# Kernel tuning notes

Hardware: AMD Instinct MI355X
Metric: run time of the kernel (lower is better)

The kernel has to match this reference:

```python
import jax, jax.numpy as jnp
import numpy as np


def _conv1x1(x, w, b):
    # x: (B, C, H, W), w: (O, C), b: (O,)  -> (B, O, H, W)
    return jnp.einsum('oc,bchw->bohw', w, x) + b[None, :, None, None]


def _branch(xq, xkv, wq, bq, wk, bk, wv, bv):
    B, C, H, W = xq.shape
    N = H * W
    q = _conv1x1(xq, wq, bq).reshape(B, -1, N)   # (B, d, N)
    k = _conv1x1(xkv, wk, bk).reshape(B, -1, N)  # (B, d, N)
    v = _conv1x1(xkv, wv, bv).reshape(B, C, N)   # (B, C, N)
    energy = jnp.einsum('bdi,bdj->bij', q, k)    # (B, N, N), no scale (as in source)
    attn = jax.nn.softmax(energy, axis=-1)
    out = jnp.einsum('bcj,bij->bci', v, attn)    # bmm(v, attn^T)
    return out.reshape(B, C, H, W)


def setup_inputs() -> dict:
    key = jax.random.key(0)
    ks = jax.random.split(key, 16)
    B, C, H, W = 4, 256, 64, 64
    d = C // 8
    s_in = 0.02
    inp = {
        'x1': jax.random.normal(ks[0], (B, C, H, W), jnp.float32),
        'x2': jax.random.normal(ks[1], (B, C, H, W), jnp.float32),
        'wq1': jax.random.normal(ks[2], (d, C), jnp.float32) * s_in,
        'bq1': jnp.zeros((d,), jnp.float32),
        'wk1': jax.random.normal(ks[3], (d, C), jnp.float32) * s_in,
        'bk1': jnp.zeros((d,), jnp.float32),
        'wv1': jax.random.normal(ks[4], (C, C), jnp.float32) * s_in,
        'bv1': jnp.zeros((C,), jnp.float32),
        'wq2': jax.random.normal(ks[5], (d, C), jnp.float32) * s_in,
        'bq2': jnp.zeros((d,), jnp.float32),
        'wk2': jax.random.normal(ks[6], (d, C), jnp.float32) * s_in,
        'bk2': jnp.zeros((d,), jnp.float32),
        'wv2': jax.random.normal(ks[7], (C, C), jnp.float32) * s_in,
        'bv2': jnp.zeros((C,), jnp.float32),
    }
    return inp


def reference(x1, x2, wq1, bq1, wk1, bk1, wv1, bv1, wq2, bq2, wk2, bk2, wv2, bv2):
    out1 = _branch(x1, x2, wq1, bq1, wk1, bk1, wv1, bv1)
    out2 = _branch(x1, x2, wq2, bq2, wk2, bk2, wv2, bv2)
    return x1 + x2 + out1 + out2
```

## Files before the change

kernel.cpp:

```cpp
#include <hip/hip_runtime.h>
#include <hip/hip_fp8.h>

#define N_TOK 4096
#define C_DIM 256
#define D_DIM 32

typedef float f32x4 __attribute__((ext_vector_type(4)));
typedef short short8 __attribute__((ext_vector_type(8)));
typedef unsigned short u16;
typedef unsigned char u8;
typedef long long i64;

__device__ __forceinline__ u16 f2bf(float f) {
    unsigned int u = __builtin_bit_cast(unsigned int, f);
    u += 0x7fffu + ((u >> 16) & 1u);
    return (u16)(u >> 16);
}
__device__ __forceinline__ float bf2f(u16 h) {
    unsigned int u = ((unsigned int)h) << 16;
    return __builtin_bit_cast(float, u);
}
__device__ __forceinline__ float exp2_fast(float x) {
#if __has_builtin(__builtin_amdgcn_exp2f)
    return __builtin_amdgcn_exp2f(x);
#else
    return exp2f(x);
#endif
}
template<bool HI>
__device__ __forceinline__ int pk_fp8(float a, float b, int old) {
#if __has_builtin(__builtin_amdgcn_cvt_pk_fp8_f32)
    return __builtin_amdgcn_cvt_pk_fp8_f32(a, b, old, HI);
#else
    __hip_fp8_e4m3 fa(a), fb(b);
    int v = (int)fa.__x | ((int)fb.__x << 8);
    return HI ? ((old & 0xffff) | (v << 16)) : ((old & ~0xffff) | (v & 0xffff));
#endif
}
__device__ __forceinline__ u8 f2fp8(float f) {
    return (u8)(pk_fp8<false>(f, f, 0) & 0xff);
}


__global__ __launch_bounds__(256) void qk_proj(
    const float* __restrict__ x1, const float* __restrict__ x2,
    const float* __restrict__ wq1, const float* __restrict__ bq1,
    const float* __restrict__ wk1, const float* __restrict__ bk1,
    const float* __restrict__ wq2, const float* __restrict__ bq2,
    const float* __restrict__ wk2, const float* __restrict__ bk2,
    u16* __restrict__ wsQ, u16* __restrict__ wsK)
{
    __shared__ float w_lds[32 * 256];
    const int ib = blockIdx.x;
    const int comb = blockIdx.y;
    const int b = comb & 3;
    const int branch = (comb >> 2) & 1;
    const int qk = comb >> 3;

    const float* x = qk ? x2 : x1;
    const float* w; const float* bias; u16* dst;
    if (qk == 0) { w = branch ? wq2 : wq1; bias = branch ? bq2 : bq1; dst = wsQ; }
    else         { w = branch ? wk2 : wk1; bias = branch ? bk2 : bk1; dst = wsK; }
    const int slice = branch * 4 + b;
    dst += (size_t)slice * N_TOK * D_DIM;
    const float osc = (qk == 0) ? 1.44269504088896341f : 1.0f;

    const int tid = threadIdx.x;
    for (int t = tid; t < 32 * 256; t += 256) w_lds[t] = w[t];
    __syncthreads();

    const int il = tid & 63;
    const int db = tid >> 6;
    const float* xc = x + (size_t)b * C_DIM * N_TOK + ib * 64 + il;

    float acc[8] = {0.f,0.f,0.f,0.f,0.f,0.f,0.f,0.f};
    for (int c4 = 0; c4 < 256; c4 += 4) {
        const float xv0 = xc[(size_t)(c4 + 0) * N_TOK];
        const float xv1 = xc[(size_t)(c4 + 1) * N_TOK];
        const float xv2 = xc[(size_t)(c4 + 2) * N_TOK];
        const float xv3 = xc[(size_t)(c4 + 3) * N_TOK];
#pragma unroll
        for (int mm = 0; mm < 8; ++mm) {
            const float4 wv = *(const float4*)&w_lds[(db * 8 + mm) * 256 + c4];
            acc[mm] += xv0 * wv.x + xv1 * wv.y + xv2 * wv.z + xv3 * wv.w;
        }
    }
    short8 pack;
#pragma unroll
    for (int mm = 0; mm < 8; ++mm)
        pack[mm] = (short)f2bf((acc[mm] + bias[db * 8 + mm]) * osc);
    *(short8*)(dst + (size_t)(ib * 64 + il) * D_DIM + db * 8) = pack;
}

__device__ __forceinline__ void stage_xt(u16* xtb, const float* xb, int ks,
                                         int wave, int lane)
{
    const int j  = (wave & 1) * 64 + lane;
    const int cb = (wave >> 1) * 16;
    const float* xp = xb + (size_t)(ks * 32 + cb) * N_TOK + j;
    u16 vals[16];
#pragma unroll
    for (int qq = 0; qq < 16; ++qq) vals[qq] = f2bf(xp[(size_t)qq * N_TOK]);
    const int swz = (j >> 1) & 3;
    u16* row = xtb + j * 32;
    const int c0 = cb >> 3;
    *(short8*)&row[((c0    ) ^ swz) * 8] = *(const short8*)&vals[0];
    *(short8*)&row[((c0 + 1) ^ swz) * 8] = *(const short8*)&vals[8];
}

__global__ __launch_bounds__(256, 2) void v_proj(
    const float* __restrict__ x2,
    const float* __restrict__ wv1, const float* __restrict__ bv1,
    const float* __restrict__ wv2, const float* __restrict__ bv2,
    u8* __restrict__ wsV)
{
    __shared__ __align__(16) u16 wl[128 * 256];
    __shared__ __align__(16) u16 xt[2][128 * 32];

    const int jt = blockIdx.x, ct = blockIdx.y, s = blockIdx.z;
    const int branch = s >> 2, b = s & 3;
    const float* w    = branch ? wv2 : wv1;
    const float* bias = branch ? bv2 : bv1;
    u8* dstB = wsV + (size_t)s * N_TOK * C_DIM;
    const float* xb = x2 + (size_t)b * C_DIM * N_TOK + jt * 128;

    const int tid = threadIdx.x;
    const int wave = tid >> 6, lane = tid & 63;
    const int wr = wave >> 1, wc = wave & 1;
    const int g = lane >> 4, li = lane & 15;

    {
        const int c = tid >> 1;
        const int kh = (tid & 1) * 128;
        const float* wrow = w + (size_t)(ct * 128 + c) * C_DIM + kh;
        u16* lrow = wl + c * 256;
#pragma unroll
        for (int kk = 0; kk < 128; kk += 8) {
            const float4 a0 = *(const float4*)&wrow[kk];
            const float4 a1 = *(const float4*)&wrow[kk + 4];
            u16 tmp[8] = {f2bf(a0.x), f2bf(a0.y), f2bf(a0.z), f2bf(a0.w),
                          f2bf(a1.x), f2bf(a1.y), f2bf(a1.z), f2bf(a1.w)};
            const int kc = (kh + kk) >> 3;
            *(short8*)&lrow[(kc ^ (c & 7)) * 8] = *(const short8*)tmp;
        }
    }
    stage_xt(&xt[0][0], xb, 0, wave, lane);
    __syncthreads();

    f32x4 acc[4][4];
#pragma unroll
    for (int mf = 0; mf < 4; ++mf)
#pragma unroll
        for (int nf = 0; nf < 4; ++nf) acc[mf][nf] = (f32x4){0.f, 0.f, 0.f, 0.f};

    int buf = 0;
    for (int ks = 0; ks < 8; ++ks) {
        if (ks < 7) stage_xt(&xt[buf ^ 1][0], xb, ks + 1, wave, lane);

        short8 af[4], bf[4];
#pragma unroll
        for (int mf = 0; mf < 4; ++mf) {
            const int c = wr * 64 + mf * 16 + li;
            af[mf] = *(const short8*)&wl[c * 256 + (((ks * 4 + g) ^ (li & 7)) * 8)];
        }
#pragma unroll
        for (int nf = 0; nf < 4; ++nf) {
            const int j = wc * 64 + nf * 16 + li;
            bf[nf] = *(const short8*)&xt[buf][j * 32 + ((g ^ ((j >> 1) & 3)) * 8)];
        }
        __builtin_amdgcn_s_setprio(1);
#pragma unroll
        for (int mf = 0; mf < 4; ++mf)
#pragma unroll
            for (int nf = 0; nf < 4; ++nf)
                acc[mf][nf] = __builtin_amdgcn_mfma_f32_16x16x32_bf16(
                    af[mf], bf[nf], acc[mf][nf], 0, 0, 0);
        __builtin_amdgcn_s_setprio(0);
        __syncthreads();
        buf ^= 1;
    }

#pragma unroll
    for (int mf = 0; mf < 4; ++mf) {
#pragma unroll
        for (int r = 0; r < 4; ++r) {
            const int c = ct * 128 + wr * 64 + mf * 16 + 4 * g + r;
            const float bv = bias[c];
#pragma unroll
            for (int nf = 0; nf < 4; ++nf) {
                const int j = jt * 128 + wc * 64 + nf * 16 + li;
                dstB[(size_t)(j >> 5) * 8192 + ((j >> 3) & 3) * 2048
                     + c * 8 + (j & 7)] = f2fp8(acc[mf][nf][r] + bv);
            }
        }
    }
}

__global__ __launch_bounds__(256, 4) void attn_fwd(
    const u16* __restrict__ Q, const u16* __restrict__ K,
    const u8* __restrict__ V, u16* __restrict__ O)
{
    __shared__ __align__(16) u8 vlds[2][2][4096];
    __shared__ float lscr[2][2][64][2];

    const int n  = blockIdx.x;
    const int s  = n & 7;
    const int ib = (n >> 3) & 63;
    const int ct = n >> 9;
    const u16* q = Q + (size_t)s * N_TOK * D_DIM;
    const u16* k = K + (size_t)s * N_TOK * D_DIM;
    const u8*  v = V + (size_t)s * N_TOK * C_DIM + ct * 1024;
    u16*       o = O + (size_t)s * N_TOK * C_DIM + ct * 128;

    const int tid  = threadIdx.x;
    const int wave = tid >> 6;
    const int lane = tid & 63;
    const int grp  = wave >> 1;
    const int wg   = wave & 1;
    const int g    = lane >> 4;
    const int li   = lane & 15;
    const int i0   = ib * 64 + wg * 32;
    const int jbase = grp * (N_TOK / 2);
    const int NP = N_TOK / 2 / 32;

    short8 qf[2];
    qf[0] = *(const short8*)(q + (size_t)(i0 + li) * D_DIM + 8 * g);
    qf[1] = *(const short8*)(q + (size_t)(i0 + 16 + li) * D_DIM + 8 * g);

    f32x4 acc[2][8];
#pragma unroll
    for (int it = 0; it < 2; ++it)
#pragma unroll
        for (int cf = 0; cf < 8; ++cf) acc[it][cf] = (f32x4){0.f, 0.f, 0.f, 0.f};
    float lsum[2] = {0.f, 0.f};

    {
        const u8* tile = v + (size_t)(jbase >> 5) * 8192;
#pragma unroll
        for (int ii = 0; ii < 2; ++ii) {
            const int p = wg * 2 + ii;
            __builtin_amdgcn_global_load_lds(
                (const __attribute__((address_space(1))) void*)(tile + p * 2048 + lane * 16),
                (__attribute__((address_space(3))) void*)(&vlds[grp][0][0] + p * 1024),
                16, 0, 0);
        }
    }
    __syncthreads();

    int buf = 0;
    for (int p = 0; p < NP; ++p) {
        if (p < NP - 1) {
            const u8* tile = v + (size_t)((jbase + (p + 1) * 32) >> 5) * 8192;
            u8* dst = &vlds[grp][buf ^ 1][0];
#pragma unroll
            for (int ii = 0; ii < 2; ++ii) {
                const int pc = wg * 2 + ii;
                __builtin_amdgcn_global_load_lds(
                    (const __attribute__((address_space(1))) void*)(tile + pc * 2048 + lane * 16),
                    (__attribute__((address_space(3))) void*)(dst + pc * 1024),
                    16, 0, 0);
            }
        }

        const int j0 = jbase + p * 32;
        const short8 ke = *(const short8*)(k + (size_t)(j0 + 2 * li    ) * D_DIM + 8 * g);
        const short8 ko = *(const short8*)(k + (size_t)(j0 + 2 * li + 1) * D_DIM + 8 * g);

        const f32x4 z = (f32x4){0.f, 0.f, 0.f, 0.f};
        i64 paL[2];
#pragma unroll
        for (int it = 0; it < 2; ++it) {
            f32x4 se = __builtin_amdgcn_mfma_f32_16x16x32_bf16(ke, qf[it], z, 0, 0, 0);
            f32x4 so = __builtin_amdgcn_mfma_f32_16x16x32_bf16(ko, qf[it], z, 0, 0, 0);
            float pe[4], po[4];
#pragma unroll
            for (int r = 0; r < 4; ++r) {
                pe[r] = exp2_fast(se[r]);
                po[r] = exp2_fast(so[r]);
            }
            lsum[it] += ((pe[0] + po[0]) + (pe[1] + po[1]))
                      + ((pe[2] + po[2]) + (pe[3] + po[3]));
            int w0 = pk_fp8<false>(pe[0], po[0], 0);
            w0     = pk_fp8<true >(pe[1], po[1], w0);
            int w1 = pk_fp8<false>(pe[2], po[2], 0);
            w1     = pk_fp8<true >(pe[3], po[3], w1);
            paL[it] = (i64)(((unsigned long long)(unsigned)w1 << 32) | (unsigned)w0);
        }

        const u8* vb = &vlds[grp][buf][0];
        const i64* vbL = (const i64*)(vb + g * 1024 + li * 8);
        __builtin_amdgcn_s_setprio(1);
#pragma unroll
        for (int cf = 0; cf < 8; ++cf) {
            const i64 vfL = vbL[cf * 16];
            acc[0][cf] = __builtin_amdgcn_mfma_f32_16x16x32_fp8_fp8(paL[0], vfL, acc[0][cf], 0, 0, 0);
            acc[1][cf] = __builtin_amdgcn_mfma_f32_16x16x32_fp8_fp8(paL[1], vfL, acc[1][cf], 0, 0, 0);
        }
        __builtin_amdgcn_s_setprio(0);
        __syncthreads();
        buf ^= 1;
    }

#pragma unroll
    for (int it = 0; it < 2; ++it) {
        lsum[it] += __shfl_xor(lsum[it], 16);
        lsum[it] += __shfl_xor(lsum[it], 32);
        lscr[grp][wg][lane][it] = lsum[it];
    }

    f32x4* pv = (f32x4*)&vlds[0][0][0];
#pragma unroll
    for (int it = 0; it < 2; ++it) {
        __syncthreads();
        if (grp == 1) {
#pragma unroll
            for (int cf = 0; cf < 8; ++cf)
                pv[(wg * 8 + cf) * 64 + lane] = acc[it][cf];
        }
        __syncthreads();
        if (grp == 0) {
#pragma unroll
            for (int cf = 0; cf < 8; ++cf) {
                const f32x4 o4 = pv[(wg * 8 + cf) * 64 + lane];
                acc[it][cf][0] += o4[0]; acc[it][cf][1] += o4[1];
                acc[it][cf][2] += o4[2]; acc[it][cf][3] += o4[3];
            }
        }
    }

    if (grp == 0) {
#pragma unroll
        for (int it = 0; it < 2; ++it) {
            const float linv = 1.0f / (lscr[0][wg][lane][it] + lscr[1][wg][lane][it]);
            float lr[4];
#pragma unroll
            for (int r = 0; r < 4; ++r) lr[r] = __shfl(linv, 4 * g + r);
#pragma unroll
            for (int cf = 0; cf < 8; ++cf)
#pragma unroll
                for (int r = 0; r < 4; ++r)
                    o[(size_t)(i0 + it * 16 + 4 * g + r) * C_DIM + cf * 16 + li] =
                        f2bf(acc[it][cf][r] * lr[r]);
        }
    }
}

__global__ __launch_bounds__(256) void epilogue(
    const float* __restrict__ x1, const float* __restrict__ x2,
    const u16* __restrict__ O, float* __restrict__ out)
{
    __shared__ float tl[64][65];
    const int it = blockIdx.x, ct = blockIdx.y, b = blockIdx.z;
    const int tid = threadIdx.x;
    const int cl = tid & 63, r0 = tid >> 6;

    const u16* O1 = O + (size_t)(b)     * N_TOK * C_DIM;
    const u16* O2 = O + (size_t)(4 + b) * N_TOK * C_DIM;

#pragma unroll
    for (int rr = 0; rr < 16; ++rr) {
        const int il = r0 + rr * 4;
        const size_t off = (size_t)(it * 64 + il) * C_DIM + ct * 64 + cl;
        tl[il][cl] = bf2f(O1[off]) + bf2f(O2[off]);
    }
    __syncthreads();
#pragma unroll
    for (int rr = 0; rr < 16; ++rr) {
        const int c2 = r0 + rr * 4;
        const size_t idx = ((size_t)b * C_DIM + ct * 64 + c2) * N_TOK + it * 64 + cl;
        out[idx] = x1[idx] + x2[idx] + tl[cl][c2];
    }
}

extern "C" void kernel_launch(void* const* d_in, const int* in_sizes, int n_in,
                              void* d_out, int out_size, void* d_ws, size_t ws_size,
                              hipStream_t stream)
{
    const float* x1  = (const float*)d_in[0];
    const float* x2  = (const float*)d_in[1];
    const float* wq1 = (const float*)d_in[2];
    const float* bq1 = (const float*)d_in[3];
    const float* wk1 = (const float*)d_in[4];
    const float* bk1 = (const float*)d_in[5];
    const float* wv1 = (const float*)d_in[6];
    const float* bv1 = (const float*)d_in[7];
    const float* wq2 = (const float*)d_in[8];
    const float* bq2 = (const float*)d_in[9];
    const float* wk2 = (const float*)d_in[10];
    const float* bk2 = (const float*)d_in[11];
    const float* wv2 = (const float*)d_in[12];
    const float* bv2 = (const float*)d_in[13];
    float* out = (float*)d_out;

    u16* wsQ = (u16*)d_ws;
    u16* wsK = wsQ + (size_t)8 * N_TOK * D_DIM;
    u8*  wsV = (u8*)(wsK + (size_t)8 * N_TOK * D_DIM);
    u16* wsO = (u16*)(wsV + (size_t)8 * N_TOK * C_DIM);

    qk_proj<<<dim3(64, 16), 256, 0, stream>>>(x1, x2, wq1, bq1, wk1, bk1,
                                              wq2, bq2, wk2, bk2, wsQ, wsK);
    v_proj<<<dim3(32, 2, 8), 256, 0, stream>>>(x2, wv1, bv1, wv2, bv2, wsV);
    attn_fwd<<<dim3(1024), 256, 0, stream>>>(wsQ, wsK, wsV, wsO);
    epilogue<<<dim3(64, 4, 4), 256, 0, stream>>>(x1, x2, wsO, out);
}
```

Baseline: 139.4 us.

## Software-pipeline QK scores and exp one tile ahead of PV MFMAs

Restructures the attention inner loop so the score MFMAs and exp/fp8 packing for tile p+1 are issued around the PV MFMAs for tile p, with K fragments prefetched two tiles ahead. The aim is to hide K global-load latency and let exp (transcendental ALU) work overlap matrix-core work instead of running serially. It adds a prologue and extra live registers (next K fragments, score accumulators), which may raise register pressure and lower occupancy.

```diff
diff --git a/kernel.cpp b/kernel.cpp
--- a/kernel.cpp
+++ b/kernel.cpp
@@ -238,18 +238,42 @@
         const u8* tile = v + (size_t)(jbase >> 5) * 8192;
 #pragma unroll
         for (int ii = 0; ii < 2; ++ii) {
-            const int p = wg * 2 + ii;
+            const int pc = wg * 2 + ii;
             __builtin_amdgcn_global_load_lds(
-                (const __attribute__((address_space(1))) void*)(tile + p * 2048 + lane * 16),
-                (__attribute__((address_space(3))) void*)(&vlds[grp][0][0] + p * 1024),
+                (const __attribute__((address_space(1))) void*)(tile + pc * 2048 + lane * 16),
+                (__attribute__((address_space(3))) void*)(&vlds[grp][0][0] + pc * 1024),
                 16, 0, 0);
         }
     }
+    short8 keC = *(const short8*)(k + (size_t)(jbase + 2 * li    ) * D_DIM + 8 * g);
+    short8 koC = *(const short8*)(k + (size_t)(jbase + 2 * li + 1) * D_DIM + 8 * g);
     __syncthreads();
+
+    const f32x4 z = (f32x4){0.f, 0.f, 0.f, 0.f};
+    i64 paC[2];
+#pragma unroll
+    for (int it = 0; it < 2; ++it) {
+        f32x4 se = __builtin_amdgcn_mfma_f32_16x16x32_bf16(keC, qf[it], z, 0, 0, 0);
+        f32x4 so = __builtin_amdgcn_mfma_f32_16x16x32_bf16(koC, qf[it], z, 0, 0, 0);
+        float pe[4], po[4];
+#pragma unroll
+        for (int r = 0; r < 4; ++r) { pe[r] = exp2_fast(se[r]); po[r] = exp2_fast(so[r]); }
+        lsum[it] += ((pe[0] + po[0]) + (pe[1] + po[1])) + ((pe[2] + po[2]) + (pe[3] + po[3]));
+        int w0 = pk_fp8<false>(pe[0], po[0], 0);
+        w0     = pk_fp8<true >(pe[1], po[1], w0);
+        int w1 = pk_fp8<false>(pe[2], po[2], 0);
+        w1     = pk_fp8<true >(pe[3], po[3], w1);
+        paC[it] = (i64)(((unsigned long long)(unsigned)w1 << 32) | (unsigned)w0);
+    }
+    keC = *(const short8*)(k + (size_t)(jbase + 32 + 2 * li    ) * D_DIM + 8 * g);
+    koC = *(const short8*)(k + (size_t)(jbase + 32 + 2 * li + 1) * D_DIM + 8 * g);
 
     int buf = 0;
     for (int p = 0; p < NP; ++p) {
-        if (p < NP - 1) {
+        const bool more = (p + 1 < NP);
+        short8 keN, koN;
+        f32x4 se0, so0, se1, so1;
+        if (more) {
             const u8* tile = v + (size_t)((jbase + (p + 1) * 32) >> 5) * 8192;
             u8* dst = &vlds[grp][buf ^ 1][0];
 #pragma unroll
@@ -260,43 +284,48 @@
                     (__attribute__((address_space(3))) void*)(dst + pc * 1024),
                     16, 0, 0);
             }
-        }
-
-        const int j0 = jbase + p * 32;
-        const short8 ke = *(const short8*)(k + (size_t)(j0 + 2 * li    ) * D_DIM + 8 * g);
-        const short8 ko = *(const short8*)(k + (size_t)(j0 + 2 * li + 1) * D_DIM + 8 * g);
-
-        const f32x4 z = (f32x4){0.f, 0.f, 0.f, 0.f};
-        i64 paL[2];
-#pragma unroll
-        for (int it = 0; it < 2; ++it) {
-            f32x4 se = __builtin_amdgcn_mfma_f32_16x16x32_bf16(ke, qf[it], z, 0, 0, 0);
-            f32x4 so = __builtin_amdgcn_mfma_f32_16x16x32_bf16(ko, qf[it], z, 0, 0, 0);
-            float pe[4], po[4];
-#pragma unroll
-            for (int r = 0; r < 4; ++r) {
-                pe[r] = exp2_fast(se[r]);
-                po[r] = exp2_fast(so[r]);
-            }
-            lsum[it] += ((pe[0] + po[0]) + (pe[1] + po[1]))
-                      + ((pe[2] + po[2]) + (pe[3] + po[3]));
-            int w0 = pk_fp8<false>(pe[0], po[0], 0);
-            w0     = pk_fp8<true >(pe[1], po[1], w0);
-            int w1 = pk_fp8<false>(pe[2], po[2], 0);
-            w1     = pk_fp8<true >(pe[3], po[3], w1);
-            paL[it] = (i64)(((unsigned long long)(unsigned)w1 << 32) | (unsigned)w0);
-        }
-
-        const u8* vb = &vlds[grp][buf][0];
-        const i64* vbL = (const i64*)(vb + g * 1024 + li * 8);
-        __builtin_amdgcn_s_setprio(1);
-#pragma unroll
-        for (int cf = 0; cf < 8; ++cf) {
-            const i64 vfL = vbL[cf * 16];
-            acc[0][cf] = __builtin_amdgcn_mfma_f32_16x16x32_fp8_fp8(paL[0], vfL, acc[0][cf], 0, 0, 0);
-            acc[1][cf] = __builtin_amdgcn_mfma_f32_16x16x32_fp8_fp8(paL[1], vfL, acc[1][cf], 0, 0, 0);
-        }
-        __builtin_amdgcn_s_setprio(0);
+            if (p + 2 < NP) {
+                const int j2 = jbase + (p + 2) * 32;
+                keN = *(const short8*)(k + (size_t)(j2 + 2 * li    ) * D_DIM + 8 * g);
+                koN = *(const short8*)(k + (size_t)(j2 + 2 * li + 1) * D_DIM + 8 * g);
+            }
+            se0 = __builtin_amdgcn_mfma_f32_16x16x32_bf16(keC, qf[0], z, 0, 0, 0);
+            so0 = __builtin_amdgcn_mfma_f32_16x16x32_bf16(koC, qf[0], z, 0, 0, 0);
+            se1 = __builtin_amdgcn_mfma_f32_16x16x32_bf16(keC, qf[1], z, 0, 0, 0);
+            so1 = __builtin_amdgcn_mfma_f32_16x16x32_bf16(koC, qf[1], z, 0, 0, 0);
+        }
+
+        {
+            const u8* vb = &vlds[grp][buf][0];
+            const i64* vbL = (const i64*)(vb + g * 1024 + li * 8);
+            __builtin_amdgcn_s_setprio(1);
+#pragma unroll
+            for (int cf = 0; cf < 8; ++cf) {
+                const i64 vfL = vbL[cf * 16];
+                acc[0][cf] = __builtin_amdgcn_mfma_f32_16x16x32_fp8_fp8(paC[0], vfL, acc[0][cf], 0, 0, 0);
+                acc[1][cf] = __builtin_amdgcn_mfma_f32_16x16x32_fp8_fp8(paC[1], vfL, acc[1][cf], 0, 0, 0);
+            }
+            __builtin_amdgcn_s_setprio(0);
+        }
+
+        if (more) {
+#pragma unroll
+            for (int it = 0; it < 2; ++it) {
+                const f32x4 se = it ? se1 : se0;
+                const f32x4 so = it ? so1 : so0;
+                float pe[4], po[4];
+#pragma unroll
+                for (int r = 0; r < 4; ++r) { pe[r] = exp2_fast(se[r]); po[r] = exp2_fast(so[r]); }
+                lsum[it] += ((pe[0] + po[0]) + (pe[1] + po[1]))
+                          + ((pe[2] + po[2]) + (pe[3] + po[3]));
+                int w0 = pk_fp8<false>(pe[0], po[0], 0);
+                w0     = pk_fp8<true >(pe[1], po[1], w0);
+                int w1 = pk_fp8<false>(pe[2], po[2], 0);
+                w1     = pk_fp8<true >(pe[3], po[3], w1);
+                paC[it] = (i64)(((unsigned long long)(unsigned)w1 << 32) | (unsigned)w0);
+            }
+            keC = keN; koC = koN;
+        }
         __syncthreads();
         buf ^= 1;
     }
```

Result: slower. 145.5 us (+4.3%).

## Give each wave private double-buffered V tiles and prefetch K into registers

Applied to the files above, without the earlier changes.

Each wave now has its own pair of LDS buffers and loads the whole V tile into them itself, instead of sharing a tile with its partner wave. This removes the per-iteration __syncthreads and replaces it with explicit vmcnt waits. K fragments for the next step are also loaded one iteration ahead into registers so their latency overlaps the current step's compute. The costs are twice the LDS footprint, twice the V global-to-LDS traffic per block, and a conservative vmcnt count that may stall on some of the just-issued prefetch loads.

```diff
diff --git a/kernel.cpp b/kernel.cpp
--- a/kernel.cpp
+++ b/kernel.cpp
@@ -200,7 +200,7 @@
     const u16* __restrict__ Q, const u16* __restrict__ K,
     const u8* __restrict__ V, u16* __restrict__ O)
 {
-    __shared__ __align__(16) u8 vlds[2][2][4096];
+    __shared__ __align__(16) u8 vlds[4][2][4096];
     __shared__ float lscr[2][2][64][2];
 
     const int n  = blockIdx.x;
@@ -223,6 +223,9 @@
     const int jbase = grp * (N_TOK / 2);
     const int NP = N_TOK / 2 / 32;
 
+    u8* const myv0 = &vlds[wave][0][0];
+    u8* const myv1 = &vlds[wave][1][0];
+
     short8 qf[2];
     qf[0] = *(const short8*)(q + (size_t)(i0 + li) * D_DIM + 8 * g);
     qf[1] = *(const short8*)(q + (size_t)(i0 + 16 + li) * D_DIM + 8 * g);
@@ -237,41 +240,41 @@
     {
         const u8* tile = v + (size_t)(jbase >> 5) * 8192;
 #pragma unroll
-        for (int ii = 0; ii < 2; ++ii) {
-            const int p = wg * 2 + ii;
+        for (int ii = 0; ii < 4; ++ii) {
             __builtin_amdgcn_global_load_lds(
-                (const __attribute__((address_space(1))) void*)(tile + p * 2048 + lane * 16),
-                (__attribute__((address_space(3))) void*)(&vlds[grp][0][0] + p * 1024),
+                (const __attribute__((address_space(1))) void*)(tile + ii * 2048 + lane * 16),
+                (__attribute__((address_space(3))) void*)(myv0 + ii * 1024),
                 16, 0, 0);
         }
     }
-    __syncthreads();
+    short8 keC = *(const short8*)(k + (size_t)(jbase + 2 * li    ) * D_DIM + 8 * g);
+    short8 koC = *(const short8*)(k + (size_t)(jbase + 2 * li + 1) * D_DIM + 8 * g);
 
     int buf = 0;
     for (int p = 0; p < NP; ++p) {
-        if (p < NP - 1) {
+        const bool more = (p + 1 < NP);
+        short8 keN, koN;
+        if (more) {
             const u8* tile = v + (size_t)((jbase + (p + 1) * 32) >> 5) * 8192;
-            u8* dst = &vlds[grp][buf ^ 1][0];
-#pragma unroll
-            for (int ii = 0; ii < 2; ++ii) {
-                const int pc = wg * 2 + ii;
+            u8* dst = buf ? myv0 : myv1;
+#pragma unroll
+            for (int ii = 0; ii < 4; ++ii) {
                 __builtin_amdgcn_global_load_lds(
-                    (const __attribute__((address_space(1))) void*)(tile + pc * 2048 + lane * 16),
-                    (__attribute__((address_space(3))) void*)(dst + pc * 1024),
+                    (const __attribute__((address_space(1))) void*)(tile + ii * 2048 + lane * 16),
+                    (__attribute__((address_space(3))) void*)(dst + ii * 1024),
                     16, 0, 0);
             }
-        }
-
-        const int j0 = jbase + p * 32;
-        const short8 ke = *(const short8*)(k + (size_t)(j0 + 2 * li    ) * D_DIM + 8 * g);
-        const short8 ko = *(const short8*)(k + (size_t)(j0 + 2 * li + 1) * D_DIM + 8 * g);
+            const int jn = jbase + (p + 1) * 32;
+            keN = *(const short8*)(k + (size_t)(jn + 2 * li    ) * D_DIM + 8 * g);
+            koN = *(const short8*)(k + (size_t)(jn + 2 * li + 1) * D_DIM + 8 * g);
+        }
 
         const f32x4 z = (f32x4){0.f, 0.f, 0.f, 0.f};
-        i64 paL[2];
+        i64 paC[2];
 #pragma unroll
         for (int it = 0; it < 2; ++it) {
-            f32x4 se = __builtin_amdgcn_mfma_f32_16x16x32_bf16(ke, qf[it], z, 0, 0, 0);
-            f32x4 so = __builtin_amdgcn_mfma_f32_16x16x32_bf16(ko, qf[it], z, 0, 0, 0);
+            f32x4 se = __builtin_amdgcn_mfma_f32_16x16x32_bf16(keC, qf[it], z, 0, 0, 0);
+            f32x4 so = __builtin_amdgcn_mfma_f32_16x16x32_bf16(koC, qf[it], z, 0, 0, 0);
             float pe[4], po[4];
 #pragma unroll
             for (int r = 0; r < 4; ++r) {
@@ -284,20 +287,26 @@
             w0     = pk_fp8<true >(pe[1], po[1], w0);
             int w1 = pk_fp8<false>(pe[2], po[2], 0);
             w1     = pk_fp8<true >(pe[3], po[3], w1);
-            paL[it] = (i64)(((unsigned long long)(unsigned)w1 << 32) | (unsigned)w0);
-        }
-
-        const u8* vb = &vlds[grp][buf][0];
-        const i64* vbL = (const i64*)(vb + g * 1024 + li * 8);
-        __builtin_amdgcn_s_setprio(1);
-#pragma unroll
-        for (int cf = 0; cf < 8; ++cf) {
-            const i64 vfL = vbL[cf * 16];
-            acc[0][cf] = __builtin_amdgcn_mfma_f32_16x16x32_fp8_fp8(paL[0], vfL, acc[0][cf], 0, 0, 0);
-            acc[1][cf] = __builtin_amdgcn_mfma_f32_16x16x32_fp8_fp8(paL[1], vfL, acc[1][cf], 0, 0, 0);
-        }
-        __builtin_amdgcn_s_setprio(0);
-        __syncthreads();
+            paC[it] = (i64)(((unsigned long long)(unsigned)w1 << 32) | (unsigned)w0);
+        }
+
+        if (more) asm volatile("s_waitcnt vmcnt(4)" ::: "memory");
+        else      asm volatile("s_waitcnt vmcnt(0)" ::: "memory");
+
+        {
+            const u8* vb = buf ? myv1 : myv0;
+            const i64* vbL = (const i64*)(vb + g * 1024 + li * 8);
+            __builtin_amdgcn_s_setprio(1);
+#pragma unroll
+            for (int cf = 0; cf < 8; ++cf) {
+                const i64 vfL = vbL[cf * 16];
+                acc[0][cf] = __builtin_amdgcn_mfma_f32_16x16x32_fp8_fp8(paC[0], vfL, acc[0][cf], 0, 0, 0);
+                acc[1][cf] = __builtin_amdgcn_mfma_f32_16x16x32_fp8_fp8(paC[1], vfL, acc[1][cf], 0, 0, 0);
+            }
+            __builtin_amdgcn_s_setprio(0);
+        }
+
+        if (more) { keC = keN; koC = koN; }
         buf ^= 1;
     }
 
```

After: 156.1 us. 1.12x slower.
